# Kernel optimization log

Measured on AMD Instinct MI355X. Metric: run time of the kernel, lower is better.

Reference implementation:

```python
import jax, jax.numpy as jnp
import numpy as np

N_NODES = 50000   # batch_size * n_verts
N_EDGES = 800000
D_FEAT = 128
UNITS = 256


def setup_inputs() -> dict:
    key = jax.random.key(0)
    k1, k2, k3, k4, k5 = jax.random.split(key, 5)
    features = jax.random.normal(k1, (N_NODES, D_FEAT), dtype=jnp.float32)
    edge_row = jax.random.randint(k2, (N_EDGES,), 0, N_NODES, dtype=jnp.int32)
    edge_col = jax.random.randint(k3, (N_EDGES,), 0, N_NODES, dtype=jnp.int32)
    edge_val = jax.random.uniform(k4, (N_EDGES,), dtype=jnp.float32)
    W = jax.random.normal(k5, (D_FEAT, UNITS), dtype=jnp.float32) * (1.0 / np.sqrt(D_FEAT))
    return {"features": features, "edge_row": edge_row, "edge_col": edge_col,
            "edge_val": edge_val, "W": W}


def reference(features, edge_row, edge_col, edge_val, W):
    # features: [N, F] (already the (batch*n_verts, F) layout the layer reshapes to)
    # A in COO: A[edge_row[e], edge_col[e]] = edge_val[e]
    n = features.shape[0]
    # in_degree = row-sum of A values, +1 for self loop
    in_degree = jax.ops.segment_sum(edge_val, edge_row, num_segments=n) + 1.0
    invsqrt_deg = jax.lax.rsqrt(in_degree)                       # [N]
    normalized = invsqrt_deg[:, None] * features                 # [N, F]
    # pooled = A @ normalized  (gather source rows, scale, scatter-add to dest)
    msgs = edge_val[:, None] * normalized[edge_col]              # [E, F]
    pooled = jax.ops.segment_sum(msgs, edge_row, num_segments=n) # [N, F]
    # self-loop contribution (normalized case)
    pooled = pooled + invsqrt_deg[:, None] * normalized
    # dense projection + relu
    out = jax.nn.relu(pooled @ W)                                # [N, units]
    return out
```

## Files before the change

### kernel.cpp

```cpp
#include <hip/hip_runtime.h>

constexpr int N = 50000;
constexpr int E = 800000;
constexpr int F = 128;
constexpr int U = 256;

constexpr int R      = 8;
constexpr int CAP    = 16;
constexpr int ROWCAP = R * CAP;
constexpr int EBLK   = E / 256;

typedef __attribute__((ext_vector_type(8))) short short8;
typedef __attribute__((ext_vector_type(4))) float float4v;

__device__ inline unsigned short f32_to_bf16(float x) {
    unsigned int u = __float_as_uint(x);
    unsigned int r = (u + 0x7fffu + ((u >> 16) & 1u)) >> 16;
    return (unsigned short)r;
}
__device__ inline float bf_lo(unsigned int u) { return __uint_as_float(u << 16); }
__device__ inline float bf_hi(unsigned int u) { return __uint_as_float(u & 0xffff0000u); }

__global__ __launch_bounds__(256) void hist_kernel(const int* __restrict__ erow,
                                                   const int* __restrict__ ecol,
                                                   const float* __restrict__ eval,
                                                   int* __restrict__ cnt,
                                                   int2* __restrict__ csr,
                                                   const float* __restrict__ W,
                                                   unsigned short* __restrict__ Wt) {
    if (blockIdx.x >= EBLK) {
        int idx = (blockIdx.x - EBLK) * 256 + threadIdx.x;
        int k = idx >> 8;
        int n = idx & 255;
        Wt[n * F + k] = f32_to_bf16(W[idx]);
        return;
    }
    int e   = blockIdx.x * 256 + threadIdx.x;
    int row = erow[e];
    int col = ecol[e];
    float v = eval[e];
    int rep = blockIdx.x & (R - 1);
    int rk  = atomicAdd(&cnt[row * R + rep], 1);
    if (rk < CAP)
        csr[(size_t)row * ROWCAP + rep * CAP + rk] = make_int2(col, __float_as_int(v));
}

__global__ __launch_bounds__(256) void norm_kernel(const float* __restrict__ feat,
                                                   const int* __restrict__ cnt,
                                                   int2* __restrict__ csr,
                                                   int2* __restrict__ meta,
                                                   unsigned int* __restrict__ nrm) {
    int gtid = blockIdx.x * 256 + threadIdx.x;
    int n    = gtid >> 6;
    int lane = threadIdx.x & 63;
    if (n >= N) return;

    int s = lane >> 3;
    int j = lane & 7;

    int cval = min(cnt[n * R + (lane & 7)], CAP);
    int tot = 0, myoff = 0, cs = 0;
    #pragma unroll
    for (int t = 0; t < 8; ++t) {
        int ct = __shfl(cval, t, 64);
        tot += ct;
        if (t < s) myoff += ct;
        if (t == s) cs = ct;
    }

    int2* base = csr + (size_t)n * ROWCAP;
    bool h0 = j < cs;
    bool h1 = (j + 8) < cs;
    int2 v0 = h0 ? base[s * CAP + j] : make_int2(0, 0);
    int2 v1 = h1 ? base[s * CAP + 8 + j] : make_int2(0, 0);

    float sum = (h0 ? __int_as_float(v0.y) : 0.f) + (h1 ? __int_as_float(v1.y) : 0.f);
    #pragma unroll
    for (int off = 32; off > 0; off >>= 1) sum += __shfl_xor(sum, off, 64);
    float iv_ = rsqrtf(sum + 1.0f);

    if (h0) base[myoff + j] = v0;
    if (h1) base[myoff + 8 + j] = v1;

    if (lane == 0) meta[n] = make_int2(tot, __float_as_int(iv_));

    float2 f = ((const float2*)feat)[n * 64 + lane];
    nrm[n * 64 + lane] =
        (unsigned int)f32_to_bf16(iv_ * f.x) | ((unsigned int)f32_to_bf16(iv_ * f.y) << 16);
}

__global__ __launch_bounds__(256) void gather_kernel(const int2* __restrict__ meta,
                                                     const int2* __restrict__ csr,
                                                     const unsigned int* __restrict__ nrm,
                                                     unsigned int* __restrict__ pooledb) {
    int gtid = blockIdx.x * 256 + threadIdx.x;
    int n    = gtid >> 6;
    int lane = threadIdx.x & 63;
    if (n >= N) return;

    int q = lane >> 4;
    int f = lane & 15;

    int2 m = meta[n];
    int tot = m.x;
    float iv_ = __int_as_float(m.y);

    const uint4* nrmv = (const uint4*)nrm;
    const int2*  base = csr + (size_t)n * ROWCAP;

    float acc[8] = {0.f, 0.f, 0.f, 0.f, 0.f, 0.f, 0.f, 0.f};

    if (q == 0) {
        uint4 u = nrmv[(size_t)n * 16 + f];
        acc[0] = iv_ * bf_lo(u.x); acc[1] = iv_ * bf_hi(u.x);
        acc[2] = iv_ * bf_lo(u.y); acc[3] = iv_ * bf_hi(u.y);
        acc[4] = iv_ * bf_lo(u.z); acc[5] = iv_ * bf_hi(u.z);
        acc[6] = iv_ * bf_lo(u.w); acc[7] = iv_ * bf_hi(u.w);
    }

    int e = 0;
    for (; e + 7 < tot; e += 8) {
        int2 pa = base[e + q];
        int2 pb = base[e + 4 + q];
        float va = __int_as_float(pa.y);
        float vb = __int_as_float(pb.y);
        uint4 ua = nrmv[(size_t)pa.x * 16 + f];
        uint4 ub = nrmv[(size_t)pb.x * 16 + f];
        acc[0] += va * bf_lo(ua.x); acc[1] += va * bf_hi(ua.x);
        acc[2] += va * bf_lo(ua.y); acc[3] += va * bf_hi(ua.y);
        acc[4] += va * bf_lo(ua.z); acc[5] += va * bf_hi(ua.z);
        acc[6] += va * bf_lo(ua.w); acc[7] += va * bf_hi(ua.w);
        acc[0] += vb * bf_lo(ub.x); acc[1] += vb * bf_hi(ub.x);
        acc[2] += vb * bf_lo(ub.y); acc[3] += vb * bf_hi(ub.y);
        acc[4] += vb * bf_lo(ub.z); acc[5] += vb * bf_hi(ub.z);
        acc[6] += vb * bf_lo(ub.w); acc[7] += vb * bf_hi(ub.w);
    }
    for (; e < tot; e += 4) {
        bool ok = (e + q) < tot;
        int2 p = ok ? base[e + q] : make_int2(0, 0);
        float v = __int_as_float(p.y);
        uint4 u = nrmv[(size_t)p.x * 16 + f];
        acc[0] += v * bf_lo(u.x); acc[1] += v * bf_hi(u.x);
        acc[2] += v * bf_lo(u.y); acc[3] += v * bf_hi(u.y);
        acc[4] += v * bf_lo(u.z); acc[5] += v * bf_hi(u.z);
        acc[6] += v * bf_lo(u.w); acc[7] += v * bf_hi(u.w);
    }

    #pragma unroll
    for (int i = 0; i < 8; ++i) {
        acc[i] += __shfl_xor(acc[i], 16, 64);
        acc[i] += __shfl_xor(acc[i], 32, 64);
    }

    if (q == 0) {
        uint4 o;
        o.x = (unsigned int)f32_to_bf16(acc[0]) | ((unsigned int)f32_to_bf16(acc[1]) << 16);
        o.y = (unsigned int)f32_to_bf16(acc[2]) | ((unsigned int)f32_to_bf16(acc[3]) << 16);
        o.z = (unsigned int)f32_to_bf16(acc[4]) | ((unsigned int)f32_to_bf16(acc[5]) << 16);
        o.w = (unsigned int)f32_to_bf16(acc[6]) | ((unsigned int)f32_to_bf16(acc[7]) << 16);
        ((uint4*)pooledb)[(size_t)n * 16 + f] = o;
    }
}

__global__ __launch_bounds__(256) void gemm_mfma_kernel(const unsigned short* __restrict__ Ab,
                                                        const unsigned short* __restrict__ Wt,
                                                        float* __restrict__ out) {
    __shared__ unsigned short As[16384];
    __shared__ unsigned short Bs[16384];
    const int tid = threadIdx.x;
    const int m0 = blockIdx.x * 128;
    const int n0 = blockIdx.y * 128;

    {
        const int r = tid >> 1;
        const int h = tid & 1;
        const int grow = m0 + r;
        const uint4* asrc = (grow < N) ? (const uint4*)(Ab + (size_t)grow * F) : nullptr;
        const uint4* bsrc = (const uint4*)(Wt + (size_t)(n0 + r) * F);
        #pragma unroll
        for (int j = 0; j < 8; ++j) {
            int o = h * 8 + j;
            int ks = o >> 2, quad = o & 3;
            int slot = ((ks * 8 + (r >> 4)) * 64) + (quad << 4) + (r & 15);
            uint4 av = asrc ? asrc[o] : make_uint4(0u, 0u, 0u, 0u);
            ((uint4*)As)[slot] = av;
            ((uint4*)Bs)[slot] = bsrc[o];
        }
    }
    __syncthreads();

    const int wave = tid >> 6;
    const int lane = tid & 63;
    float4v acc[8][2];
    #pragma unroll
    for (int i = 0; i < 8; ++i) {
        acc[i][0] = (float4v){0.f, 0.f, 0.f, 0.f};
        acc[i][1] = (float4v){0.f, 0.f, 0.f, 0.f};
    }

    #pragma unroll
    for (int ks = 0; ks < 4; ++ks) {
        short8 b0 = *(const short8*)&Bs[(((ks * 8 + wave * 2 + 0) * 64) + lane) * 8];
        short8 b1 = *(const short8*)&Bs[(((ks * 8 + wave * 2 + 1) * 64) + lane) * 8];
        #pragma unroll
        for (int mt = 0; mt < 8; ++mt) {
            short8 a = *(const short8*)&As[(((ks * 8 + mt) * 64) + lane) * 8];
            acc[mt][0] = __builtin_amdgcn_mfma_f32_16x16x32_bf16(a, b0, acc[mt][0], 0, 0, 0);
            acc[mt][1] = __builtin_amdgcn_mfma_f32_16x16x32_bf16(a, b1, acc[mt][1], 0, 0, 0);
        }
    }

    const int quad = lane >> 4;
    const int colt = lane & 15;
    #pragma unroll
    for (int mt = 0; mt < 8; ++mt) {
        #pragma unroll
        for (int nt = 0; nt < 2; ++nt) {
            int col = n0 + (wave * 2 + nt) * 16 + colt;
            #pragma unroll
            for (int i = 0; i < 4; ++i) {
                int row = m0 + mt * 16 + quad * 4 + i;
                if (row < N) out[(size_t)row * U + col] = fmaxf(acc[mt][nt][i], 0.f);
            }
        }
    }
}

extern "C" void kernel_launch(void* const* d_in, const int* in_sizes, int n_in,
                              void* d_out, int out_size, void* d_ws, size_t ws_size,
                              hipStream_t stream) {
    (void)in_sizes; (void)n_in; (void)out_size; (void)ws_size;

    const float* feat = (const float*)d_in[0];
    const int*   erow = (const int*)d_in[1];
    const int*   ecol = (const int*)d_in[2];
    const float* eval = (const float*)d_in[3];
    const float* W    = (const float*)d_in[4];
    float* out = (float*)d_out;

    char* ws = (char*)d_ws;
    int*            cnt     = (int*)  (ws + 0);
    int2*           meta    = (int2*) (ws + 1600000);
    unsigned short* Wt      = (unsigned short*)(ws + 2000000);
    unsigned int*   nrm     = (unsigned int*)  (ws + 2065536);
    unsigned int*   pooledb = (unsigned int*)  (ws + 14865536);
    int2*           csr     = (int2*) (ws + 27665536);

    (void)hipMemsetAsync(cnt, 0, (size_t)N * R * sizeof(int), stream);

    hist_kernel<<<EBLK + (F * U) / 256, 256, 0, stream>>>(erow, ecol, eval, cnt, csr, W, Wt);
    norm_kernel  <<<(N * 64) / 256, 256, 0, stream>>>(feat, cnt, csr, meta, nrm);
    gather_kernel<<<(N * 64) / 256, 256, 0, stream>>>(meta, csr, nrm, pooledb);

    dim3 ggrid((N + 127) / 128, U / 128);
    gemm_mfma_kernel<<<ggrid, 256, 0, stream>>>((const unsigned short*)pooledb, Wt, out);
}
```

Measured before the change: 205.3 us.

## Fuse neighbor gather with MFMA projection and drop the pooled intermediate

Merges the gather and GEMM kernels into one. Each 256-thread block aggregates 16 node rows into shared memory as bf16, then runs MFMA against W read straight from global memory, with ReLU applied on the output. This removes the pooled bf16 buffer round trip through global memory and one kernel launch. In exchange each block computes only a 16-row tile, so W is reloaded from global/L2 by every block, and the GEMM phase waits on the slowest gather row in the block.

Result: no change. 205.3 us (+0.0%).

```diff
diff --git a/kernel.cpp b/kernel.cpp
--- a/kernel.cpp
+++ b/kernel.cpp
@@ -9,6 +9,8 @@
 constexpr int CAP    = 16;
 constexpr int ROWCAP = R * CAP;
 constexpr int EBLK   = E / 256;
+
+constexpr int PLD = 136;
 
 typedef __attribute__((ext_vector_type(8))) short short8;
 typedef __attribute__((ext_vector_type(4))) float float4v;
@@ -89,139 +91,107 @@
         (unsigned int)f32_to_bf16(iv_ * f.x) | ((unsigned int)f32_to_bf16(iv_ * f.y) << 16);
 }
 
-__global__ __launch_bounds__(256) void gather_kernel(const int2* __restrict__ meta,
-                                                     const int2* __restrict__ csr,
-                                                     const unsigned int* __restrict__ nrm,
-                                                     unsigned int* __restrict__ pooledb) {
-    int gtid = blockIdx.x * 256 + threadIdx.x;
-    int n    = gtid >> 6;
-    int lane = threadIdx.x & 63;
-    if (n >= N) return;
-
-    int q = lane >> 4;
-    int f = lane & 15;
-
-    int2 m = meta[n];
-    int tot = m.x;
-    float iv_ = __int_as_float(m.y);
-
+__global__ __launch_bounds__(256) void gather_gemm_kernel(const int2* __restrict__ meta,
+                                                          const int2* __restrict__ csr,
+                                                          const unsigned int* __restrict__ nrm,
+                                                          const unsigned short* __restrict__ Wt,
+                                                          float* __restrict__ out) {
+    __shared__ unsigned short plds[16 * PLD];
+    const int tid  = threadIdx.x;
+    const int w    = tid >> 6;
+    const int lane = tid & 63;
+    const int q    = lane >> 4;
+    const int f    = lane & 15;
     const uint4* nrmv = (const uint4*)nrm;
-    const int2*  base = csr + (size_t)n * ROWCAP;
-
-    float acc[8] = {0.f, 0.f, 0.f, 0.f, 0.f, 0.f, 0.f, 0.f};
-
-    if (q == 0) {
-        uint4 u = nrmv[(size_t)n * 16 + f];
-        acc[0] = iv_ * bf_lo(u.x); acc[1] = iv_ * bf_hi(u.x);
-        acc[2] = iv_ * bf_lo(u.y); acc[3] = iv_ * bf_hi(u.y);
-        acc[4] = iv_ * bf_lo(u.z); acc[5] = iv_ * bf_hi(u.z);
-        acc[6] = iv_ * bf_lo(u.w); acc[7] = iv_ * bf_hi(u.w);
-    }
-
-    int e = 0;
-    for (; e + 7 < tot; e += 8) {
-        int2 pa = base[e + q];
-        int2 pb = base[e + 4 + q];
-        float va = __int_as_float(pa.y);
-        float vb = __int_as_float(pb.y);
-        uint4 ua = nrmv[(size_t)pa.x * 16 + f];
-        uint4 ub = nrmv[(size_t)pb.x * 16 + f];
-        acc[0] += va * bf_lo(ua.x); acc[1] += va * bf_hi(ua.x);
-        acc[2] += va * bf_lo(ua.y); acc[3] += va * bf_hi(ua.y);
-        acc[4] += va * bf_lo(ua.z); acc[5] += va * bf_hi(ua.z);
-        acc[6] += va * bf_lo(ua.w); acc[7] += va * bf_hi(ua.w);
-        acc[0] += vb * bf_lo(ub.x); acc[1] += vb * bf_hi(ub.x);
-        acc[2] += vb * bf_lo(ub.y); acc[3] += vb * bf_hi(ub.y);
-        acc[4] += vb * bf_lo(ub.z); acc[5] += vb * bf_hi(ub.z);
-        acc[6] += vb * bf_lo(ub.w); acc[7] += vb * bf_hi(ub.w);
-    }
-    for (; e < tot; e += 4) {
-        bool ok = (e + q) < tot;
-        int2 p = ok ? base[e + q] : make_int2(0, 0);
-        float v = __int_as_float(p.y);
-        uint4 u = nrmv[(size_t)p.x * 16 + f];
-        acc[0] += v * bf_lo(u.x); acc[1] += v * bf_hi(u.x);
-        acc[2] += v * bf_lo(u.y); acc[3] += v * bf_hi(u.y);
-        acc[4] += v * bf_lo(u.z); acc[5] += v * bf_hi(u.z);
-        acc[6] += v * bf_lo(u.w); acc[7] += v * bf_hi(u.w);
-    }
-
-    #pragma unroll
-    for (int i = 0; i < 8; ++i) {
-        acc[i] += __shfl_xor(acc[i], 16, 64);
-        acc[i] += __shfl_xor(acc[i], 32, 64);
-    }
-
-    if (q == 0) {
-        uint4 o;
-        o.x = (unsigned int)f32_to_bf16(acc[0]) | ((unsigned int)f32_to_bf16(acc[1]) << 16);
-        o.y = (unsigned int)f32_to_bf16(acc[2]) | ((unsigned int)f32_to_bf16(acc[3]) << 16);
-        o.z = (unsigned int)f32_to_bf16(acc[4]) | ((unsigned int)f32_to_bf16(acc[5]) << 16);
-        o.w = (unsigned int)f32_to_bf16(acc[6]) | ((unsigned int)f32_to_bf16(acc[7]) << 16);
-        ((uint4*)pooledb)[(size_t)n * 16 + f] = o;
-    }
-}
-
-__global__ __launch_bounds__(256) void gemm_mfma_kernel(const unsigned short* __restrict__ Ab,
-                                                        const unsigned short* __restrict__ Wt,
-                                                        float* __restrict__ out) {
-    __shared__ unsigned short As[16384];
-    __shared__ unsigned short Bs[16384];
-    const int tid = threadIdx.x;
-    const int m0 = blockIdx.x * 128;
-    const int n0 = blockIdx.y * 128;
-
-    {
-        const int r = tid >> 1;
-        const int h = tid & 1;
-        const int grow = m0 + r;
-        const uint4* asrc = (grow < N) ? (const uint4*)(Ab + (size_t)grow * F) : nullptr;
-        const uint4* bsrc = (const uint4*)(Wt + (size_t)(n0 + r) * F);
+
+    #pragma unroll
+    for (int i = 0; i < 4; ++i) {
+        int ridx = w * 4 + i;
+        int n    = blockIdx.x * 16 + ridx;
+        int2 m   = meta[n];
+        int tot  = m.x;
+        float iv_ = __int_as_float(m.y);
+        const int2* base = csr + (size_t)n * ROWCAP;
+
+        float acc[8] = {0.f, 0.f, 0.f, 0.f, 0.f, 0.f, 0.f, 0.f};
+
+        if (q == 0) {
+            uint4 u = nrmv[(size_t)n * 16 + f];
+            acc[0] = iv_ * bf_lo(u.x); acc[1] = iv_ * bf_hi(u.x);
+            acc[2] = iv_ * bf_lo(u.y); acc[3] = iv_ * bf_hi(u.y);
+            acc[4] = iv_ * bf_lo(u.z); acc[5] = iv_ * bf_hi(u.z);
+            acc[6] = iv_ * bf_lo(u.w); acc[7] = iv_ * bf_hi(u.w);
+        }
+
+        int e = 0;
+        for (; e + 7 < tot; e += 8) {
+            int2 pa = base[e + q];
+            int2 pb = base[e + 4 + q];
+            float va = __int_as_float(pa.y);
+            float vb = __int_as_float(pb.y);
+            uint4 ua = nrmv[(size_t)pa.x * 16 + f];
+            uint4 ub = nrmv[(size_t)pb.x * 16 + f];
+            acc[0] += va * bf_lo(ua.x); acc[1] += va * bf_hi(ua.x);
+            acc[2] += va * bf_lo(ua.y); acc[3] += va * bf_hi(ua.y);
+            acc[4] += va * bf_lo(ua.z); acc[5] += va * bf_hi(ua.z);
+            acc[6] += va * bf_lo(ua.w); acc[7] += va * bf_hi(ua.w);
+            acc[0] += vb * bf_lo(ub.x); acc[1] += vb * bf_hi(ub.x);
+            acc[2] += vb * bf_lo(ub.y); acc[3] += vb * bf_hi(ub.y);
+            acc[4] += vb * bf_lo(ub.z); acc[5] += vb * bf_hi(ub.z);
+            acc[6] += vb * bf_lo(ub.w); acc[7] += vb * bf_hi(ub.w);
+        }
+        for (; e < tot; e += 4) {
+            bool ok = (e + q) < tot;
+            int2 p = ok ? base[e + q] : make_int2(0, 0);
+            float v = __int_as_float(p.y);
+            uint4 u = nrmv[(size_t)p.x * 16 + f];
+            acc[0] += v * bf_lo(u.x); acc[1] += v * bf_hi(u.x);
+            acc[2] += v * bf_lo(u.y); acc[3] += v * bf_hi(u.y);
+            acc[4] += v * bf_lo(u.z); acc[5] += v * bf_hi(u.z);
+            acc[6] += v * bf_lo(u.w); acc[7] += v * bf_hi(u.w);
+        }
+
         #pragma unroll
-        for (int j = 0; j < 8; ++j) {
-            int o = h * 8 + j;
-            int ks = o >> 2, quad = o & 3;
-            int slot = ((ks * 8 + (r >> 4)) * 64) + (quad << 4) + (r & 15);
-            uint4 av = asrc ? asrc[o] : make_uint4(0u, 0u, 0u, 0u);
-            ((uint4*)As)[slot] = av;
-            ((uint4*)Bs)[slot] = bsrc[o];
+        for (int k = 0; k < 8; ++k) {
+            acc[k] += __shfl_xor(acc[k], 16, 64);
+            acc[k] += __shfl_xor(acc[k], 32, 64);
+        }
+
+        if (q == 0) {
+            uint4 o;
+            o.x = (unsigned int)f32_to_bf16(acc[0]) | ((unsigned int)f32_to_bf16(acc[1]) << 16);
+            o.y = (unsigned int)f32_to_bf16(acc[2]) | ((unsigned int)f32_to_bf16(acc[3]) << 16);
+            o.z = (unsigned int)f32_to_bf16(acc[4]) | ((unsigned int)f32_to_bf16(acc[5]) << 16);
+            o.w = (unsigned int)f32_to_bf16(acc[6]) | ((unsigned int)f32_to_bf16(acc[7]) << 16);
+            *(uint4*)&plds[ridx * PLD + f * 8] = o;
         }
     }
     __syncthreads();
 
-    const int wave = tid >> 6;
-    const int lane = tid & 63;
-    float4v acc[8][2];
-    #pragma unroll
-    for (int i = 0; i < 8; ++i) {
-        acc[i][0] = (float4v){0.f, 0.f, 0.f, 0.f};
-        acc[i][1] = (float4v){0.f, 0.f, 0.f, 0.f};
-    }
+    float4v gacc[4];
+    #pragma unroll
+    for (int t = 0; t < 4; ++t) gacc[t] = (float4v){0.f, 0.f, 0.f, 0.f};
 
     #pragma unroll
     for (int ks = 0; ks < 4; ++ks) {
-        short8 b0 = *(const short8*)&Bs[(((ks * 8 + wave * 2 + 0) * 64) + lane) * 8];
-        short8 b1 = *(const short8*)&Bs[(((ks * 8 + wave * 2 + 1) * 64) + lane) * 8];
+        short8 a = *(const short8*)&plds[(lane & 15) * PLD + ks * 32 + (lane >> 4) * 8];
         #pragma unroll
-        for (int mt = 0; mt < 8; ++mt) {
-            short8 a = *(const short8*)&As[(((ks * 8 + mt) * 64) + lane) * 8];
-            acc[mt][0] = __builtin_amdgcn_mfma_f32_16x16x32_bf16(a, b0, acc[mt][0], 0, 0, 0);
-            acc[mt][1] = __builtin_amdgcn_mfma_f32_16x16x32_bf16(a, b1, acc[mt][1], 0, 0, 0);
+        for (int t = 0; t < 4; ++t) {
+            int col = (w * 4 + t) * 16 + (lane & 15);
+            short8 b = *(const short8*)&Wt[(size_t)col * F + ks * 32 + (lane >> 4) * 8];
+            gacc[t] = __builtin_amdgcn_mfma_f32_16x16x32_bf16(a, b, gacc[t], 0, 0, 0);
         }
     }
 
     const int quad = lane >> 4;
     const int colt = lane & 15;
     #pragma unroll
-    for (int mt = 0; mt < 8; ++mt) {
+    for (int t = 0; t < 4; ++t) {
+        int col = (w * 4 + t) * 16 + colt;
         #pragma unroll
-        for (int nt = 0; nt < 2; ++nt) {
-            int col = n0 + (wave * 2 + nt) * 16 + colt;
-            #pragma unroll
-            for (int i = 0; i < 4; ++i) {
-                int row = m0 + mt * 16 + quad * 4 + i;
-                if (row < N) out[(size_t)row * U + col] = fmaxf(acc[mt][nt][i], 0.f);
-            }
+        for (int i = 0; i < 4; ++i) {
+            int row = blockIdx.x * 16 + quad * 4 + i;
+            out[(size_t)row * U + col] = fmaxf(gacc[t][i], 0.f);
         }
     }
 }
@@ -239,19 +209,15 @@
     float* out = (float*)d_out;
 
     char* ws = (char*)d_ws;
-    int*            cnt     = (int*)  (ws + 0);
-    int2*           meta    = (int2*) (ws + 1600000);
-    unsigned short* Wt      = (unsigned short*)(ws + 2000000);
-    unsigned int*   nrm     = (unsigned int*)  (ws + 2065536);
-    unsigned int*   pooledb = (unsigned int*)  (ws + 14865536);
-    int2*           csr     = (int2*) (ws + 27665536);
+    int*            cnt  = (int*)  (ws + 0);
+    int2*           meta = (int2*) (ws + 1601536);
+    unsigned short* Wt   = (unsigned short*)(ws + 2001536);
+    unsigned int*   nrm  = (unsigned int*)  (ws + 2067072);
+    int2*           csr  = (int2*) (ws + 14867072);
 
     (void)hipMemsetAsync(cnt, 0, (size_t)N * R * sizeof(int), stream);
 
     hist_kernel<<<EBLK + (F * U) / 256, 256, 0, stream>>>(erow, ecol, eval, cnt, csr, W, Wt);
-    norm_kernel  <<<(N * 64) / 256, 256, 0, stream>>>(feat, cnt, csr, meta, nrm);
-    gather_kernel<<<(N * 64) / 256, 256, 0, stream>>>(meta, csr, nrm, pooledb);
-
-    dim3 ggrid((N + 127) / 128, U / 128);
-    gemm_mfma_kernel<<<ggrid, 256, 0, stream>>>((const unsigned short*)pooledb, Wt, out);
-}
+    norm_kernel<<<(N * 64) / 256, 256, 0, stream>>>(feat, cnt, csr, meta, nrm);
+    gather_gemm_kernel<<<N / 16, 256, 0, stream>>>(meta, csr, nrm, Wt, out);
+}
```
